# Kernel tuning notes

Hardware: AMD Instinct MI355X
Metric: run time of the kernel (lower is better)

## Reference

```python
import jax, jax.numpy as jnp
import numpy as np


def conv3d(x, w, b):
    # x: [B,C,D,H,W], w: [O,I,3,3,3], padding=1, stride=1
    y = jax.lax.conv_general_dilated(
        x, w, window_strides=(1, 1, 1), padding=[(1, 1)] * 3,
        dimension_numbers=("NCDHW", "OIDHW", "NCDHW"))
    return y + b[None, :, None, None, None]


def trilinear_sample(x, cd, ch, cw):
    # x: [B,C,D,H,W]; cd/ch/cw: [B,K,D,H,W] float sampling coords.
    # Zero padding outside the volume (invalid corners masked to 0).
    B, C, D, H, W = x.shape
    d0 = jnp.floor(cd); h0 = jnp.floor(ch); w0 = jnp.floor(cw)
    fd, fh, fw = cd - d0, ch - h0, cw - w0
    d0 = d0.astype(jnp.int32); h0 = h0.astype(jnp.int32); w0 = w0.astype(jnp.int32)
    gather = jax.vmap(lambda xb, z, y, xx: xb[:, z, y, xx])  # -> [B,C,K,D,H,W]
    out = jnp.zeros((B, C) + cd.shape[1:], x.dtype)
    for dz in (0, 1):
        wz = fd if dz else 1.0 - fd
        zi = d0 + dz
        for dy in (0, 1):
            wy = fh if dy else 1.0 - fh
            yi = h0 + dy
            for dx in (0, 1):
                wx = fw if dx else 1.0 - fw
                xi = w0 + dx
                valid = ((zi >= 0) & (zi < D) & (yi >= 0) & (yi < H)
                         & (xi >= 0) & (xi < W)).astype(x.dtype)
                v = gather(x, jnp.clip(zi, 0, D - 1), jnp.clip(yi, 0, H - 1),
                           jnp.clip(xi, 0, W - 1))
                out = out + (wz * wy * wx * valid)[:, None] * v
    return out


def deform_conv3d(x, offsets, mask, w, b):
    # Modulated deformable 3D conv (DCNv2-style), kernel 3x3x3, pad 1, stride 1.
    # offsets: [B,81,D,H,W] = 27 taps x (dd,dh,dw); mask: [B,27,D,H,W].
    B, C, D, H, W = x.shape
    K = 27
    off = offsets.reshape(B, K, 3, D, H, W)
    kd, kh, kw = jnp.meshgrid(jnp.arange(3), jnp.arange(3), jnp.arange(3), indexing="ij")
    tap_d = (kd.reshape(-1) - 1).astype(x.dtype)[None, :, None, None, None]
    tap_h = (kh.reshape(-1) - 1).astype(x.dtype)[None, :, None, None, None]
    tap_w = (kw.reshape(-1) - 1).astype(x.dtype)[None, :, None, None, None]
    gd = jnp.arange(D, dtype=x.dtype)[None, None, :, None, None]
    gh = jnp.arange(H, dtype=x.dtype)[None, None, None, :, None]
    gw = jnp.arange(W, dtype=x.dtype)[None, None, None, None, :]
    cd = gd + tap_d + off[:, :, 0]
    ch = gh + tap_h + off[:, :, 1]
    cw = gw + tap_w + off[:, :, 2]
    sampled = trilinear_sample(x, cd, ch, cw) * mask[:, None]  # [B,C,K,D,H,W]
    out = jnp.einsum("bckdhw,ock->bodhw", sampled, w.reshape(w.shape[0], C, K))
    return out + b[None, :, None, None, None]


def mdconv3d(x, ow, ob, w, b):
    # MDConv3d: internal offset/mask predictor + modulated deformable conv.
    d = conv3d(x, ow, ob)
    offsets, mask = d[:, :81], jax.nn.sigmoid(d[:, 81:])
    return deform_conv3d(x, offsets, mask, w, b)


def forward(x, ow1, ob1, w1, b1, ow2, ob2, w2, b2, ow3, ob3, w3, b3,
            defo_w, defo_b, c3d_w, c3d_b):
    h = jax.nn.relu(mdconv3d(x, ow1, ob1, w1, b1))
    h = jax.nn.relu(mdconv3d(h, ow2, ob2, w2, b2))
    h = jax.nn.relu(mdconv3d(h, ow3, ob3, w3, b3))
    d = conv3d(h, defo_w, defo_b)
    offsets, alpha = d[:, :81], jax.nn.sigmoid(d[:, 81:])
    return deform_conv3d(x, offsets, alpha, c3d_w, c3d_b)


def setup_inputs() -> dict:
    key = jax.random.key(0)
    ks = jax.random.split(key, 16)
    B, C, D, H, W = 1, 256, 8, 32, 32
    M = 256  # mdim
    OFF_SCALE = 0.02  # small init so predicted offsets stay moderate

    def p(k, shape):
        return jax.random.normal(k, shape, jnp.float32) * OFF_SCALE

    inp = {"x": jax.random.normal(ks[0], (B, C, D, H, W), jnp.float32)}
    c_ins = [C, M, M]
    for i, cin in enumerate(c_ins, 1):
        inp[f"ow{i}"] = p(ks[2 * i - 1], (108, cin, 3, 3, 3))
        inp[f"ob{i}"] = jnp.zeros((108,), jnp.float32)
        inp[f"w{i}"] = p(ks[2 * i], (M, cin, 3, 3, 3))
        inp[f"b{i}"] = jnp.zeros((M,), jnp.float32)
    inp["defo_w"] = p(ks[13], (108, M, 3, 3, 3))
    inp["defo_b"] = jnp.zeros((108,), jnp.float32)
    inp["c3d_w"] = p(ks[14], (256, C, 3, 3, 3))
    inp["c3d_b"] = jnp.zeros((256,), jnp.float32)
    return inp


def reference(x, ow1, ob1, w1, b1, ow2, ob2, w2, b2, ow3, ob3, w3, b3,
              defo_w, defo_b, c3d_w, c3d_b):
    return forward(x, ow1, ob1, w1, b1, ow2, ob2, w2, b2, ow3, ob3, w3, b3,
                   defo_w, defo_b, c3d_w, c3d_b)
```

## Files before the change

### kernel.cpp

```cpp
#include <hip/hip_runtime.h>
#include <cstdint>

#define NPOS 8192
#define KTOT 6912
#define XP_ROWS 11560
#define XP_SY 34
#define XP_SZ 1156
#define KS 4
#define KSL 1728
#define NCHUNK 27

typedef float  facc_t __attribute__((ext_vector_type(4)));
typedef short  bf8_t  __attribute__((ext_vector_type(8)));
typedef unsigned short ub8_t __attribute__((ext_vector_type(8)));

__device__ __forceinline__ unsigned short f2bf(float f) {
    unsigned u = __float_as_uint(f);
    u = (u + 0x7FFFu + ((u >> 16) & 1u)) >> 16;
    return (unsigned short)u;
}
__device__ __forceinline__ float bf2f(unsigned short u) {
    return __uint_as_float(((unsigned)u) << 16);
}

__global__ __launch_bounds__(256) void zero_k(unsigned short* __restrict__ dst) {
    ub8_t zz = {0,0,0,0,0,0,0,0};
    *(ub8_t*)&dst[((size_t)blockIdx.x * 256 + threadIdx.x) * 8] = zz;
}

__global__ __launch_bounds__(256) void pad_x_t(const float* __restrict__ x,
                                               unsigned short* __restrict__ XpA) {
    __shared__ unsigned short T[256 * 33];
    int b = blockIdx.x;
    int z = b >> 5, y = b & 31;
    int t = threadIdx.x;
    int c8 = t >> 5, xv = t & 31;
#pragma unroll 4
    for (int i = 0; i < 32; ++i) {
        int c = i * 8 + c8;
        T[c * 33 + xv] = f2bf(x[c * NPOS + (z << 10) + (y << 5) + xv]);
    }
    __syncthreads();
    int rowb = ((z + 1) * XP_SZ + (y + 1) * XP_SY + 1) * 256;
#pragma unroll 4
    for (int j = 0; j < 32; ++j) {
        XpA[rowb + j * 256 + t] = T[t * 33 + j];
    }
}

__global__ __launch_bounds__(256) void wtrans_all(
    const float* __restrict__ o1, const float* __restrict__ o2,
    const float* __restrict__ o3, const float* __restrict__ o4,
    const float* __restrict__ m1, const float* __restrict__ m2,
    const float* __restrict__ m3, const float* __restrict__ m4,
    unsigned short* __restrict__ wtoff, unsigned short* __restrict__ wtmain) {
    __shared__ float T[6912];
    int b = blockIdx.x, t = threadIdx.x;
    const float* src; unsigned short* dst; int o, O;
    if (b < 512) {
        int L = b >> 7; o = b & 127; O = 108;
        src = (L == 0) ? o1 : (L == 1) ? o2 : (L == 2) ? o3 : o4;
        dst = wtoff + ((size_t)(L * 128 + o)) * KTOT;
    } else {
        int b2 = b - 512;
        int L = b2 >> 8; o = b2 & 255; O = 256;
        src = (L == 0) ? m1 : (L == 1) ? m2 : (L == 2) ? m3 : m4;
        dst = wtmain + ((size_t)(L * 256 + o)) * KTOT;
    }
    if (o < O) {
#pragma unroll 3
        for (int i = 0; i < 27; ++i) T[i * 256 + t] = src[(size_t)o * KTOT + i * 256 + t];
        __syncthreads();
#pragma unroll 3
        for (int i = 0; i < 27; ++i) {
            int kc = i * 256 + t;
            int c = kc & 255, k = kc >> 8;
            dst[kc] = f2bf(T[c * 27 + k]);
        }
    } else {
#pragma unroll 3
        for (int i = 0; i < 27; ++i) dst[i * 256 + t] = 0;
    }
}

template<bool DEFORM>
__global__ __launch_bounds__(256)
void fgemm(const unsigned short* __restrict__ Xp,
           const unsigned short* __restrict__ wt,
           const float* __restrict__ dbuf,
           float* __restrict__ parts) {
    constexpr int O   = DEFORM ? 256 : 128;
    constexpr int PWN = DEFORM ? 4 : 2;
    __shared__ unsigned short Bs[64 * 64] __attribute__((aligned(16)));

    const int t = threadIdx.x;
    const int wave = t >> 6, lane = t & 63;
    const int q = lane >> 4, r = lane & 15;

    const int bid = blockIdx.x + (blockIdx.y << 7);
    const int xcd = bid & 7;
    const int idx = bid >> 3;
    const int pt  = (xcd << 4) | (idx & 15);
    const int ks  = idx >> 4;
    const int pbase = pt * 64;
    const int kstart = ks * KSL;

    const int obw = DEFORM ? (wave * 64) : ((wave >> 1) * 64);
    const int pfb = DEFORM ? 0 : ((wave & 1) * 32);

    const int pl = t >> 2;
    const int csub = (t & 3) * 16;
    const int p = pbase + pl;
    const int z = p >> 10, y = (p >> 5) & 31, xx = p & 31;
    const int g0 = (t & 3) * 2;
    const int wr0 = pl * 64 + ((g0 ^ (pl & 7)) << 3);
    const int wr1 = pl * 64 + (((g0 + 1) ^ (pl & 7)) << 3);

    facc_t acc[4][PWN];
#pragma unroll
    for (int i = 0; i < 4; ++i)
#pragma unroll
        for (int ip = 0; ip < PWN; ++ip) acc[i][ip] = (facc_t){0.f, 0.f, 0.f, 0.f};

    float cw[8];
    int row0 = 0;
    int kprev = -1;

    for (int chunk = 0; chunk < NCHUNK; ++chunk) {
        const int kc0 = kstart + chunk * 64;
        const int k = kc0 >> 8;
        const int c0 = kc0 & 255;
        const int kd = k / 9, kh = (k / 3) % 3, kw = k % 3;

        bf8_t afr[2][4];
#pragma unroll
        for (int sl = 0; sl < 2; ++sl)
#pragma unroll
            for (int i = 0; i < 4; ++i)
                afr[sl][i] = *(const bf8_t*)&wt[(size_t)(obw + i * 16 + r) * KTOT + kc0 + sl * 32 + q * 8];

        if (DEFORM) {
            if (k != kprev) {
                kprev = k;
                float od  = dbuf[(3 * k + 0) * NPOS + p];
                float oh  = dbuf[(3 * k + 1) * NPOS + p];
                float ow_ = dbuf[(3 * k + 2) * NPOS + p];
                float m   = dbuf[(81 + k) * NPOS + p];
                float cd = (float)(z + kd - 1) + od;
                float ch = (float)(y + kh - 1) + oh;
                float cx = (float)(xx + kw - 1) + ow_;
                float fdf = floorf(cd), fhf = floorf(ch), fwf = floorf(cx);
                float fd = cd - fdf, fh = ch - fhf, fw = cx - fwf;
                float wz0 = 1.f - fd, wz1 = fd;
                float wy0 = 1.f - fh, wy1 = fh;
                float wx0 = 1.f - fw, wx1 = fw;
                int id, ih, iw;
                if (fdf < -1.f || fdf >= 8.f)  { wz0 = 0.f; wz1 = 0.f; id = 0; } else id = (int)fdf;
                if (fhf < -1.f || fhf >= 32.f) { wy0 = 0.f; wy1 = 0.f; ih = 0; } else ih = (int)fhf;
                if (fwf < -1.f || fwf >= 32.f) { wx0 = 0.f; wx1 = 0.f; iw = 0; } else iw = (int)fwf;
                wz0 *= m; wz1 *= m;
                float w00 = wz0 * wy0, w01 = wz0 * wy1, w10 = wz1 * wy0, w11 = wz1 * wy1;
                cw[0] = w00 * wx0; cw[1] = w00 * wx1;
                cw[2] = w01 * wx0; cw[3] = w01 * wx1;
                cw[4] = w10 * wx0; cw[5] = w10 * wx1;
                cw[6] = w11 * wx0; cw[7] = w11 * wx1;
                row0 = (id + 1) * XP_SZ + (ih + 1) * XP_SY + (iw + 1);
            }
            float av[16];
#pragma unroll
            for (int e = 0; e < 16; ++e) av[e] = 0.f;
            const unsigned short* cb = Xp + (size_t)row0 * 256 + c0 + csub;
#pragma unroll
            for (int j = 0; j < 8; ++j) {
                const int roff = ((j >> 2) & 1) * XP_SZ + ((j >> 1) & 1) * XP_SY + (j & 1);
                ub8_t lo = *(const ub8_t*)(cb + roff * 256);
                ub8_t hi = *(const ub8_t*)(cb + roff * 256 + 8);
#pragma unroll
                for (int e = 0; e < 8; ++e) {
                    av[e]     += cw[j] * bf2f(lo[e]);
                    av[8 + e] += cw[j] * bf2f(hi[e]);
                }
            }
            ub8_t v0, v1;
#pragma unroll
            for (int e = 0; e < 8; ++e) { v0[e] = f2bf(av[e]); v1[e] = f2bf(av[8 + e]); }
            *(ub8_t*)&Bs[wr0] = v0;
            *(ub8_t*)&Bs[wr1] = v1;
        } else {
            int row = (z + kd) * XP_SZ + (y + kh) * XP_SY + (xx + kw);
            ub8_t lo = *(const ub8_t*)&Xp[(size_t)row * 256 + c0 + csub];
            ub8_t hi = *(const ub8_t*)&Xp[(size_t)row * 256 + c0 + csub + 8];
            *(ub8_t*)&Bs[wr0] = lo;
            *(ub8_t*)&Bs[wr1] = hi;
        }
        __syncthreads();

#pragma unroll
        for (int sl = 0; sl < 2; ++sl) {
            bf8_t bfr[PWN];
#pragma unroll
            for (int ip = 0; ip < PWN; ++ip) {
                int brow = pfb + ip * 16 + r;
                bfr[ip] = *(const bf8_t*)&Bs[brow * 64 + (((sl * 4 + q) ^ (brow & 7)) << 3)];
            }
#pragma unroll
            for (int i = 0; i < 4; ++i)
#pragma unroll
                for (int ip = 0; ip < PWN; ++ip)
                    acc[i][ip] = __builtin_amdgcn_mfma_f32_16x16x32_bf16(afr[sl][i], bfr[ip], acc[i][ip], 0, 0, 0);
        }
        __syncthreads();
    }

    float* pp = parts + (size_t)ks * O * NPOS;
#pragma unroll
    for (int i = 0; i < 4; ++i)
#pragma unroll
        for (int ip = 0; ip < PWN; ++ip)
#pragma unroll
            for (int reg = 0; reg < 4; ++reg) {
                int o = obw + i * 16 + q * 4 + reg;
                int px = pbase + pfb + ip * 16 + r;
                pp[(size_t)o * NPOS + px] = acc[i][ip][reg];
            }
}

__global__ __launch_bounds__(256) void ccombine(const float* __restrict__ parts,
                                                const float* __restrict__ ob,
                                                float* __restrict__ dbuf) {
    int b = blockIdx.x;
    int o = b >> 3;
    int p4 = ((b & 7) * 256 + threadIdx.x) * 4;
    float s0 = 0, s1 = 0, s2 = 0, s3 = 0;
#pragma unroll
    for (int s = 0; s < KS; ++s) {
        const float4 v = *(const float4*)&parts[((size_t)(s * 128 + o)) * NPOS + p4];
        s0 += v.x; s1 += v.y; s2 += v.z; s3 += v.w;
    }
    float bv = ob[o];
    s0 += bv; s1 += bv; s2 += bv; s3 += bv;
    if (o >= 81) {
        s0 = 1.f / (1.f + __expf(-s0));
        s1 = 1.f / (1.f + __expf(-s1));
        s2 = 1.f / (1.f + __expf(-s2));
        s3 = 1.f / (1.f + __expf(-s3));
    }
    *(float4*)&dbuf[(size_t)o * NPOS + p4] = make_float4(s0, s1, s2, s3);
}

__global__ __launch_bounds__(256) void dcombine_h(const float* __restrict__ parts,
                                                  const float* __restrict__ bias,
                                                  unsigned short* __restrict__ XpB) {
    __shared__ unsigned short T[64 * 66];
    int p0 = blockIdx.x * 64, o0 = blockIdx.y * 64;
    int t = threadIdx.x;
    int pl = t & 63, og = t >> 6;
#pragma unroll 4
    for (int j = 0; j < 16; ++j) {
        int ol = og * 16 + j;
        float s = 0.f;
#pragma unroll
        for (int sp = 0; sp < KS; ++sp)
            s += parts[((size_t)(sp * 256 + o0 + ol)) * NPOS + p0 + pl];
        s += bias[o0 + ol];
        T[ol * 66 + pl] = f2bf(fmaxf(s, 0.f));
    }
    __syncthreads();
    int c = t & 63, pr = t >> 6;
#pragma unroll 4
    for (int j = 0; j < 16; ++j) {
        int pl2 = j * 4 + pr;
        int pg = p0 + pl2;
        int zz = pg >> 10, yy = (pg >> 5) & 31, xv = pg & 31;
        int row = (zz + 1) * XP_SZ + (yy + 1) * XP_SY + xv + 1;
        XpB[(size_t)row * 256 + o0 + c] = T[c * 66 + pl2];
    }
}

__global__ __launch_bounds__(256) void dcombine_out(const float* __restrict__ parts,
                                                    const float* __restrict__ bias,
                                                    float* __restrict__ out) {
    int b = blockIdx.x;
    int o = b >> 3;
    int p4 = ((b & 7) * 256 + threadIdx.x) * 4;
    float s0 = 0, s1 = 0, s2 = 0, s3 = 0;
#pragma unroll
    for (int s = 0; s < KS; ++s) {
        const float4 v = *(const float4*)&parts[((size_t)(s * 256 + o)) * NPOS + p4];
        s0 += v.x; s1 += v.y; s2 += v.z; s3 += v.w;
    }
    float bv = bias[o];
    *(float4*)&out[(size_t)o * NPOS + p4] = make_float4(s0 + bv, s1 + bv, s2 + bv, s3 + bv);
}

extern "C" void kernel_launch(void* const* d_in, const int* in_sizes, int n_in,
                              void* d_out, int out_size, void* d_ws, size_t ws_size,
                              hipStream_t stream) {
    const float* x      = (const float*)d_in[0];
    const float* ow1    = (const float*)d_in[1];
    const float* ob1    = (const float*)d_in[2];
    const float* w1     = (const float*)d_in[3];
    const float* b1     = (const float*)d_in[4];
    const float* ow2    = (const float*)d_in[5];
    const float* ob2    = (const float*)d_in[6];
    const float* w2     = (const float*)d_in[7];
    const float* b2     = (const float*)d_in[8];
    const float* ow3    = (const float*)d_in[9];
    const float* ob3    = (const float*)d_in[10];
    const float* w3     = (const float*)d_in[11];
    const float* b3     = (const float*)d_in[12];
    const float* defo_w = (const float*)d_in[13];
    const float* defo_b = (const float*)d_in[14];
    const float* c3d_w  = (const float*)d_in[15];
    const float* c3d_b  = (const float*)d_in[16];
    float* out = (float*)d_out;

    unsigned short* XpA    = (unsigned short*)d_ws;
    unsigned short* XpB    = XpA + (size_t)XP_ROWS * 256;
    unsigned short* wtoff  = XpB + (size_t)XP_ROWS * 256;
    unsigned short* wtmain = wtoff + (size_t)4 * 128 * KTOT;
    float* dbufp = (float*)(wtmain + (size_t)4 * 256 * KTOT);
    float* parts = dbufp + (size_t)108 * NPOS;

    const dim3 blk(256);
    const dim3 gG(128, KS);

    zero_k<<<2890, blk, 0, stream>>>(XpA);
    pad_x_t<<<256, blk, 0, stream>>>(x, XpA);
    wtrans_all<<<1536, blk, 0, stream>>>(ow1, ow2, ow3, defo_w, w1, w2, w3, c3d_w, wtoff, wtmain);

    const float* cbias[4] = {ob1, ob2, ob3, defo_b};
    const float* dbias[4] = {b1, b2, b3, c3d_b};

    for (int L = 0; L < 4; ++L) {
        const unsigned short* featConv = (L == 0) ? XpA : XpB;
        const unsigned short* featDef  = (L == 3) ? XpA : featConv;
        fgemm<false><<<gG, blk, 0, stream>>>(featConv, wtoff + (size_t)L * 128 * KTOT, nullptr, parts);
        ccombine<<<864, blk, 0, stream>>>(parts, cbias[L], dbufp);
        fgemm<true><<<gG, blk, 0, stream>>>(featDef, wtmain + (size_t)L * 256 * KTOT, dbufp, parts);
        if (L < 3) dcombine_h<<<dim3(128, 4), blk, 0, stream>>>(parts, dbias[L], XpB);
        else       dcombine_out<<<2048, blk, 0, stream>>>(parts, dbias[L], out);
    }
}
```

Measured before the change: 766.6 us.

## Prefetch next chunk's deformable gather loads during current chunk in fgemm

The deformable path now issues the eight-corner global gathers for the next K chunk into a 16-register staging array before the current chunk's MFMA phase, so load latency overlaps compute. Full __syncthreads are replaced by a raw s_barrier with an explicit lgkmcnt wait and sched_barrier, so the barrier does not wait on the outstanding global prefetch loads. Launch bounds add a minimum of two blocks per CU. This raises register pressure and depends on the barrier and LDS wait ordering staying correct.

Result: faster. 742.2 us (-3.2%).

```diff
diff --git a/kernel.cpp b/kernel.cpp
--- a/kernel.cpp
+++ b/kernel.cpp
@@ -84,7 +84,7 @@
 }
 
 template<bool DEFORM>
-__global__ __launch_bounds__(256)
+__global__ __launch_bounds__(256, 2)
 void fgemm(const unsigned short* __restrict__ Xp,
            const unsigned short* __restrict__ wt,
            const float* __restrict__ dbuf,
@@ -125,6 +125,48 @@
     float cw[8];
     int row0 = 0;
     int kprev = -1;
+    ub8_t stv[16];
+
+    auto prep_issue = [&](int kc0_s) {
+        const int k_s = kc0_s >> 8;
+        const int c0_s = kc0_s & 255;
+        if (k_s != kprev) {
+            kprev = k_s;
+            const int kd = k_s / 9, kh = (k_s / 3) % 3, kw = k_s % 3;
+            float od  = dbuf[(3 * k_s + 0) * NPOS + p];
+            float oh  = dbuf[(3 * k_s + 1) * NPOS + p];
+            float ow_ = dbuf[(3 * k_s + 2) * NPOS + p];
+            float m   = dbuf[(81 + k_s) * NPOS + p];
+            float cd = (float)(z + kd - 1) + od;
+            float ch = (float)(y + kh - 1) + oh;
+            float cx = (float)(xx + kw - 1) + ow_;
+            float fdf = floorf(cd), fhf = floorf(ch), fwf = floorf(cx);
+            float fd = cd - fdf, fh = ch - fhf, fw = cx - fwf;
+            float wz0 = 1.f - fd, wz1 = fd;
+            float wy0 = 1.f - fh, wy1 = fh;
+            float wx0 = 1.f - fw, wx1 = fw;
+            int id, ih, iw;
+            if (fdf < -1.f || fdf >= 8.f)  { wz0 = 0.f; wz1 = 0.f; id = 0; } else id = (int)fdf;
+            if (fhf < -1.f || fhf >= 32.f) { wy0 = 0.f; wy1 = 0.f; ih = 0; } else ih = (int)fhf;
+            if (fwf < -1.f || fwf >= 32.f) { wx0 = 0.f; wx1 = 0.f; iw = 0; } else iw = (int)fwf;
+            wz0 *= m; wz1 *= m;
+            float w00 = wz0 * wy0, w01 = wz0 * wy1, w10 = wz1 * wy0, w11 = wz1 * wy1;
+            cw[0] = w00 * wx0; cw[1] = w00 * wx1;
+            cw[2] = w01 * wx0; cw[3] = w01 * wx1;
+            cw[4] = w10 * wx0; cw[5] = w10 * wx1;
+            cw[6] = w11 * wx0; cw[7] = w11 * wx1;
+            row0 = (id + 1) * XP_SZ + (ih + 1) * XP_SY + (iw + 1);
+        }
+        const unsigned short* cb = Xp + (size_t)row0 * 256 + c0_s + csub;
+#pragma unroll
+        for (int j = 0; j < 8; ++j) {
+            const int roff = ((j >> 2) & 1) * XP_SZ + ((j >> 1) & 1) * XP_SY + (j & 1);
+            stv[2 * j]     = *(const ub8_t*)(cb + roff * 256);
+            stv[2 * j + 1] = *(const ub8_t*)(cb + roff * 256 + 8);
+        }
+    };
+
+    if (DEFORM) prep_issue(kstart);
 
     for (int chunk = 0; chunk < NCHUNK; ++chunk) {
         const int kc0 = kstart + chunk * 64;
@@ -140,50 +182,21 @@
                 afr[sl][i] = *(const bf8_t*)&wt[(size_t)(obw + i * 16 + r) * KTOT + kc0 + sl * 32 + q * 8];
 
         if (DEFORM) {
-            if (k != kprev) {
-                kprev = k;
-                float od  = dbuf[(3 * k + 0) * NPOS + p];
-                float oh  = dbuf[(3 * k + 1) * NPOS + p];
-                float ow_ = dbuf[(3 * k + 2) * NPOS + p];
-                float m   = dbuf[(81 + k) * NPOS + p];
-                float cd = (float)(z + kd - 1) + od;
-                float ch = (float)(y + kh - 1) + oh;
-                float cx = (float)(xx + kw - 1) + ow_;
-                float fdf = floorf(cd), fhf = floorf(ch), fwf = floorf(cx);
-                float fd = cd - fdf, fh = ch - fhf, fw = cx - fwf;
-                float wz0 = 1.f - fd, wz1 = fd;
-                float wy0 = 1.f - fh, wy1 = fh;
-                float wx0 = 1.f - fw, wx1 = fw;
-                int id, ih, iw;
-                if (fdf < -1.f || fdf >= 8.f)  { wz0 = 0.f; wz1 = 0.f; id = 0; } else id = (int)fdf;
-                if (fhf < -1.f || fhf >= 32.f) { wy0 = 0.f; wy1 = 0.f; ih = 0; } else ih = (int)fhf;
-                if (fwf < -1.f || fwf >= 32.f) { wx0 = 0.f; wx1 = 0.f; iw = 0; } else iw = (int)fwf;
-                wz0 *= m; wz1 *= m;
-                float w00 = wz0 * wy0, w01 = wz0 * wy1, w10 = wz1 * wy0, w11 = wz1 * wy1;
-                cw[0] = w00 * wx0; cw[1] = w00 * wx1;
-                cw[2] = w01 * wx0; cw[3] = w01 * wx1;
-                cw[4] = w10 * wx0; cw[5] = w10 * wx1;
-                cw[6] = w11 * wx0; cw[7] = w11 * wx1;
-                row0 = (id + 1) * XP_SZ + (ih + 1) * XP_SY + (iw + 1);
-            }
             float av[16];
 #pragma unroll
             for (int e = 0; e < 16; ++e) av[e] = 0.f;
-            const unsigned short* cb = Xp + (size_t)row0 * 256 + c0 + csub;
 #pragma unroll
             for (int j = 0; j < 8; ++j) {
-                const int roff = ((j >> 2) & 1) * XP_SZ + ((j >> 1) & 1) * XP_SY + (j & 1);
-                ub8_t lo = *(const ub8_t*)(cb + roff * 256);
-                ub8_t hi = *(const ub8_t*)(cb + roff * 256 + 8);
 #pragma unroll
                 for (int e = 0; e < 8; ++e) {
-                    av[e]     += cw[j] * bf2f(lo[e]);
-                    av[8 + e] += cw[j] * bf2f(hi[e]);
+                    av[e]     += cw[j] * bf2f(stv[2 * j][e]);
+                    av[8 + e] += cw[j] * bf2f(stv[2 * j + 1][e]);
                 }
             }
             ub8_t v0, v1;
 #pragma unroll
             for (int e = 0; e < 8; ++e) { v0[e] = f2bf(av[e]); v1[e] = f2bf(av[8 + e]); }
+            if (chunk + 1 < NCHUNK) prep_issue(kc0 + 64);
             *(ub8_t*)&Bs[wr0] = v0;
             *(ub8_t*)&Bs[wr1] = v1;
         } else {
@@ -193,7 +206,10 @@
             *(ub8_t*)&Bs[wr0] = lo;
             *(ub8_t*)&Bs[wr1] = hi;
         }
-        __syncthreads();
+
+        asm volatile("s_waitcnt lgkmcnt(0)" ::: "memory");
+        __builtin_amdgcn_s_barrier();
+        __builtin_amdgcn_sched_barrier(0);
 
 #pragma unroll
         for (int sl = 0; sl < 2; ++sl) {
@@ -209,7 +225,9 @@
                 for (int ip = 0; ip < PWN; ++ip)
                     acc[i][ip] = __builtin_amdgcn_mfma_f32_16x16x32_bf16(afr[sl][i], bfr[ip], acc[i][ip], 0, 0, 0);
         }
-        __syncthreads();
+
+        __builtin_amdgcn_s_barrier();
+        __builtin_amdgcn_sched_barrier(0);
     }
 
     float* pp = parts + (size_t)ks * O * NPOS;
```
